# Kernel optimization log

Hardware: AMD Instinct MI355X
Metric: run time of the kernel (lower is better)

## Reference

```python
import jax, jax.numpy as jnp
import numpy as np

N_DOMAIN = 10
DOM_EMB = 4
IN_DIM = 1024
HIDDEN = [1024, 512, 256]
N_EXPERTS = 8
LORA_R = 16


def _glorot(key, shape):
    fan_in, fan_out = shape[-2], shape[-1]
    lim = np.sqrt(6.0 / (fan_in + fan_out))
    return jax.random.uniform(key, shape, jnp.float32, -lim, lim)


def setup_inputs() -> dict:
    key = jax.random.key(0)
    ks = jax.random.split(key, 32)
    inp = {
        "dnn_input": jax.random.normal(ks[0], (16384, IN_DIM), jnp.float32),
        "domain_input": jax.random.randint(ks[1], (16384,), 0, N_DOMAIN, jnp.int64),
        "emb_table": jax.random.normal(ks[2], (N_DOMAIN, DOM_EMB), jnp.float32),
        "gate_W": _glorot(ks[3], (DOM_EMB, N_EXPERTS)),
        "gate_b": jnp.zeros((N_EXPERTS,), jnp.float32),
    }
    prev = IN_DIM
    k = 4
    for li, h in enumerate(HIDDEN):
        inp[f"W{li}"] = _glorot(ks[k], (prev, h)); k += 1
        inp[f"b{li}"] = jnp.zeros((h,), jnp.float32)
        # original inits B and lora_bias to zeros; use small randoms so outputs/grads are non-trivial
        inp[f"A{li}"] = _glorot(ks[k], (N_EXPERTS, prev, LORA_R)); k += 1
        inp[f"B{li}"] = 0.01 * jax.random.normal(ks[k], (N_EXPERTS, LORA_R, h), jnp.float32); k += 1
        inp[f"lb{li}"] = 0.01 * jax.random.normal(ks[k], (N_EXPERTS, h), jnp.float32); k += 1
        prev = h
    return inp


def _moe_layer(x, gate, W, b, A, B, lb):
    # base GEMM (dropout is identity: rate 0 / inference)
    base = x @ W + b                                   # [B, h]
    t = jnp.einsum('bp,epr->ber', x, A)                # [B, E, r]
    eo = jnp.einsum('ber,erh->beh', t, B) + lb[None]   # [B, E, h]
    moe = jnp.einsum('be,beh->bh', gate, eo)           # [B, h]
    return jax.nn.relu(base + moe)


def reference(dnn_input, domain_input, emb_table, gate_W, gate_b,
              W0, b0, A0, B0, lb0,
              W1, b1, A1, B1, lb1,
              W2, b2, A2, B2, lb2):
    dom = emb_table[domain_input]                      # [B, 4]
    gate = jax.nn.softmax(dom @ gate_W + gate_b, axis=-1)  # [B, E]
    x = dnn_input
    x = _moe_layer(x, gate, W0, b0, A0, B0, lb0)
    x = _moe_layer(x, gate, W1, b1, A1, B1, lb1)
    x = _moe_layer(x, gate, W2, b2, A2, B2, lb2)
    return x
```

## Files before the change

### kernel.cpp

```cpp
#include <hip/hip_runtime.h>
#include <hip/hip_bf16.h>
#include <stdint.h>

#define KAUG 192
#define M_ROWS 16384

typedef __attribute__((ext_vector_type(8))) __bf16 bf16x8;
typedef __attribute__((ext_vector_type(4))) float f32x4;

__device__ __forceinline__ unsigned short f2b(float f) {
  unsigned int u = __builtin_bit_cast(unsigned int, f);
  u = (u + 0x7fffu + ((u >> 16) & 1u)) >> 16;
  return (unsigned short)u;
}

__device__ __forceinline__ void lds_load16(const unsigned short* g, unsigned short* l) {
  __builtin_amdgcn_global_load_lds(
      (const __attribute__((address_space(1))) void*)g,
      (__attribute__((address_space(3))) void*)l, 16, 0, 0);
}

template<int N> __device__ __forceinline__ void vmcnt_wait() {
  if constexpr (N == 0)      asm volatile("s_waitcnt vmcnt(0)" ::: "memory");
  else if constexpr (N == 3) asm volatile("s_waitcnt vmcnt(3)" ::: "memory");
  else if constexpr (N == 4) asm volatile("s_waitcnt vmcnt(4)" ::: "memory");
  else if constexpr (N == 6) asm volatile("s_waitcnt vmcnt(6)" ::: "memory");
  else                       asm volatile("s_waitcnt vmcnt(8)" ::: "memory");
}


__global__ void gate_aug_kernel(const int* __restrict__ dom, const float* __restrict__ emb,
                                const float* __restrict__ gW, const float* __restrict__ gb,
                                float* __restrict__ gate, unsigned short* __restrict__ tg) {
  int i = blockIdx.x * blockDim.x + threadIdx.x;
  int d = dom[i];
  float e0 = emb[d*4+0], e1 = emb[d*4+1], e2 = emb[d*4+2], e3 = emb[d*4+3];
  float l[8]; float mx = -1e30f;
#pragma unroll
  for (int j = 0; j < 8; j++) {
    l[j] = e0*gW[j] + e1*gW[8+j] + e2*gW[16+j] + e3*gW[24+j] + gb[j];
    mx = fmaxf(mx, l[j]);
  }
  float s = 0.f;
#pragma unroll
  for (int j = 0; j < 8; j++) { l[j] = __expf(l[j] - mx); s += l[j]; }
  float inv = 1.0f / s;
  unsigned int g[4];
#pragma unroll
  for (int j = 0; j < 8; j++) {
    float v = l[j] * inv;
    gate[i*8+j] = v;
    unsigned int b = f2b(v);
    if (j & 1) g[j >> 1] |= b << 16; else g[j >> 1] = b;
  }
  uint4* dst = (uint4*)&tg[(long)i * KAUG + 128];
  dst[0] = make_uint4(g[0], g[1], g[2], g[3]);
  uint4 z4 = make_uint4(0, 0, 0, 0);
#pragma unroll
  for (int q = 1; q < 8; q++) dst[q] = z4;
}

__global__ void build_wt_all(const float* __restrict__ w0, const float* __restrict__ w1,
                             const float* __restrict__ w2,
                             unsigned short* __restrict__ t0, unsigned short* __restrict__ t1,
                             unsigned short* __restrict__ t2) {
  int z = blockIdx.z;
  const float* W = z == 0 ? w0 : (z == 1 ? w1 : w2);
  unsigned short* Wt = z == 0 ? t0 : (z == 1 ? t1 : t2);
  int K = (z == 2) ? 512 : 1024;
  int N = (z == 0) ? 1024 : (z == 1 ? 512 : 256);
  int n0 = blockIdx.x * 32, k0 = blockIdx.y * 32;
  if (n0 >= N || k0 >= K) return;
  __shared__ float tl[32][33];
  int tx = threadIdx.x & 31, ty = threadIdx.x >> 5;
#pragma unroll
  for (int i = 0; i < 32; i += 8)
    tl[ty + i][tx] = W[(long)(k0 + ty + i) * N + n0 + tx];
  __syncthreads();
#pragma unroll
  for (int i = 0; i < 32; i += 8)
    Wt[(long)(n0 + ty + i) * K + k0 + tx] = f2b(tl[tx][ty + i]);
}

__global__ void build_aft_all(const float* __restrict__ a0, const float* __restrict__ a1,
                              const float* __restrict__ a2,
                              unsigned short* __restrict__ t0, unsigned short* __restrict__ t1,
                              unsigned short* __restrict__ t2) {
  int z = blockIdx.z;
  const float* A = z == 0 ? a0 : (z == 1 ? a1 : a2);
  unsigned short* Aft = z == 0 ? t0 : (z == 1 ? t1 : t2);
  int P = (z == 2) ? 512 : 1024;
  long p0 = (long)blockIdx.x * 64;
  if (p0 >= P) return;
  int e = blockIdx.y;
  __shared__ float tl[64][17];
  int t = threadIdx.x;
#pragma unroll
  for (int pass = 0; pass < 4; pass++) {
    int idx = t + pass * 256;
    int pl = idx >> 4, r = idx & 15;
    tl[pl][r] = A[((long)e * P + p0 + pl) * 16 + r];
  }
  __syncthreads();
#pragma unroll
  for (int pass = 0; pass < 4; pass++) {
    int idx = t + pass * 256;
    int r = idx >> 6, pl = idx & 63;
    Aft[(long)(e * 16 + r) * P + p0 + pl] = f2b(tl[pl][r]);
  }
}

__global__ void build_bft_all(const float* __restrict__ b0, const float* __restrict__ b1,
                              const float* __restrict__ b2,
                              const float* __restrict__ l0, const float* __restrict__ l1,
                              const float* __restrict__ l2,
                              unsigned short* __restrict__ t0, unsigned short* __restrict__ t1,
                              unsigned short* __restrict__ t2) {
  int z = blockIdx.z;
  const float* Bm = z == 0 ? b0 : (z == 1 ? b1 : b2);
  const float* lb = z == 0 ? l0 : (z == 1 ? l1 : l2);
  unsigned short* Bft = z == 0 ? t0 : (z == 1 ? t1 : t2);
  int H = (z == 0) ? 1024 : (z == 1 ? 512 : 256);
  int n0 = blockIdx.x * 32, kk0 = blockIdx.y * 32;
  if (n0 >= H) return;
  __shared__ float tl[32][33];
  int tx = threadIdx.x & 31, ty = threadIdx.x >> 5;
#pragma unroll
  for (int i = 0; i < 32; i += 8) {
    int kk = kk0 + ty + i;
    float v;
    if (kk < 128)       v = Bm[(long)kk * H + n0 + tx];
    else if (kk < 136)  v = lb[(long)(kk - 128) * H + n0 + tx];
    else                v = 0.f;
    tl[ty + i][tx] = v;
  }
  __syncthreads();
#pragma unroll
  for (int i = 0; i < 32; i += 8)
    Bft[(long)(n0 + ty + i) * KAUG + kk0 + tx] = f2b(tl[tx][ty + i]);
}

template<int MODE, int BM>
__global__ __launch_bounds__(512)
void gemm_mn(const unsigned short* __restrict__ A1, int lda1, int K1,
             const unsigned short* __restrict__ A2, int lda2, int K2,
             const unsigned short* __restrict__ Bt1, int ldb1,
             const unsigned short* __restrict__ Bt2, int ldb2,
             const float* __restrict__ bias,
             const float* __restrict__ gate,
             void* __restrict__ outp, int ldout) {
  constexpr int MFRAG = BM / 32;
  constexpr int ATOT = BM * 64;
  constexpr int BTOT = 128 * 64;
  constexpr int LA = BM / 64;
  constexpr int L = LA + 2;
  __shared__ __attribute__((aligned(16))) unsigned short lds[3 * ATOT + 3 * BTOT];

  const int t = threadIdx.x;
  const int lane = t & 63, wave = t >> 6;
  const int wr = wave >> 2, wc = wave & 3;
  const int rl = lane & 15, kg = lane >> 4;
  const int row0 = blockIdx.x * BM, col0 = blockIdx.y * 128;

  const int sr = t >> 3;
  const int sk = ((t & 7) ^ (sr & 7)) * 8;

  f32x4 acc[MFRAG][2];
#pragma unroll
  for (int m = 0; m < MFRAG; m++)
#pragma unroll
    for (int n = 0; n < 2; n++) acc[m][n] = (f32x4){0.f, 0.f, 0.f, 0.f};

  auto stageA = [&](int buf, int kt) {
    const unsigned short* src; long ld; int kl;
    if (kt < K1) { src = A1; ld = lda1; kl = kt; }
    else         { src = A2; ld = lda2; kl = kt - K1; }
    unsigned short* d = &lds[buf * ATOT + t * 8];
    const unsigned short* s = src + (long)(row0 + sr) * ld + kl + sk;
#pragma unroll
    for (int i = 0; i < LA; i++)
      lds_load16(s + (long)(i * 64) * ld, d + i * 4096);
  };
  auto stageB = [&](int buf, int kt) {
    const unsigned short* src; long ld; int kl;
    if (kt < K1) { src = Bt1; ld = ldb1; kl = kt; }
    else         { src = Bt2; ld = ldb2; kl = kt - K1; }
    unsigned short* d = &lds[3 * ATOT + buf * BTOT + t * 8];
    const unsigned short* s = src + (long)(col0 + sr) * ld + kl + sk;
    lds_load16(s, d);
    lds_load16(s + 64 * ld, d + 4096);
  };
  auto ldA = [&](int buf, int mg, int ks) {
    int lr = wr * (BM / 2) + mg * 16 + rl;
    int sc = (ks * 4 + kg) ^ (lr & 7);
    return *(const bf16x8*)&lds[buf * ATOT + lr * 64 + sc * 8];
  };
  auto ldB = [&](int buf, int n, int ks) {
    int cr = wc * 32 + n * 16 + rl;
    int sc = (ks * 4 + kg) ^ (cr & 7);
    return *(const bf16x8*)&lds[3 * ATOT + buf * BTOT + cr * 64 + sc * 8];
  };

  const int Ktot = K1 + K2;
  const int NT = Ktot / 64;

  stageA(0, 0); stageB(0, 0);
  stageA(1, 64); stageB(1, 64);
  vmcnt_wait<L>();
  __builtin_amdgcn_s_barrier();

  int bcur = 0;
  bf16x8 Bfv[2][2];
  for (int tt = 0; tt < NT; ++tt) {
    int bpf = bcur + 2; if (bpf > 2) bpf -= 3;
    const bool pf = (tt + 2 < NT);
    bf16x8 Af[(MFRAG + 1) / 2][2];
#pragma unroll
    for (int m = 0; m < MFRAG / 2; m++) { Af[m][0] = ldA(bcur, m, 0); Af[m][1] = ldA(bcur, m, 1); }
#pragma unroll
    for (int n = 0; n < 2; n++) { Bfv[n][0] = ldB(bcur, n, 0); Bfv[n][1] = ldB(bcur, n, 1); }
    if (pf) stageA(bpf, (tt + 2) * 64);
    __builtin_amdgcn_s_barrier();
    asm volatile("s_waitcnt lgkmcnt(0)" ::: "memory");
    __builtin_amdgcn_sched_barrier(0);
    __builtin_amdgcn_s_setprio(1);
#pragma unroll
    for (int m = 0; m < MFRAG / 2; m++)
#pragma unroll
      for (int n = 0; n < 2; n++) {
        acc[m][n] = __builtin_amdgcn_mfma_f32_16x16x32_bf16(Af[m][0], Bfv[n][0], acc[m][n], 0, 0, 0);
        acc[m][n] = __builtin_amdgcn_mfma_f32_16x16x32_bf16(Af[m][1], Bfv[n][1], acc[m][n], 0, 0, 0);
      }
    __builtin_amdgcn_s_setprio(0);
    __builtin_amdgcn_s_barrier();
#pragma unroll
    for (int m = 0; m < MFRAG / 2; m++) { Af[m][0] = ldA(bcur, MFRAG / 2 + m, 0); Af[m][1] = ldA(bcur, MFRAG / 2 + m, 1); }
    if (pf) stageB(bpf, (tt + 2) * 64);
    if (tt + 1 < NT) vmcnt_wait<L>();
    else             vmcnt_wait<0>();
    __builtin_amdgcn_s_barrier();
    asm volatile("s_waitcnt lgkmcnt(0)" ::: "memory");
    __builtin_amdgcn_sched_barrier(0);
    __builtin_amdgcn_s_setprio(1);
#pragma unroll
    for (int m = 0; m < MFRAG / 2; m++)
#pragma unroll
      for (int n = 0; n < 2; n++) {
        acc[MFRAG / 2 + m][n] = __builtin_amdgcn_mfma_f32_16x16x32_bf16(Af[m][0], Bfv[n][0], acc[MFRAG / 2 + m][n], 0, 0, 0);
        acc[MFRAG / 2 + m][n] = __builtin_amdgcn_mfma_f32_16x16x32_bf16(Af[m][1], Bfv[n][1], acc[MFRAG / 2 + m][n], 0, 0, 0);
      }
    __builtin_amdgcn_s_setprio(0);
    __builtin_amdgcn_s_barrier();
    bcur = bcur == 2 ? 0 : bcur + 1;
  }

#pragma unroll
  for (int m = 0; m < MFRAG; m++)
#pragma unroll
    for (int n = 0; n < 2; n++)
#pragma unroll
      for (int j = 0; j < 4; j++) {
        int row = row0 + wr * (BM / 2) + m * 16 + kg * 4 + j;
        int col = col0 + wc * 32 + n * 16 + rl;
        float v = acc[m][n][j];
        if (MODE == 0) {
          v *= gate[row * 8 + (col >> 4)];
          ((unsigned short*)outp)[(long)row * ldout + col] = f2b(v);
        } else {
          v += bias[col];
          v = fmaxf(v, 0.f);
          if (MODE == 1) ((unsigned short*)outp)[(long)row * ldout + col] = f2b(v);
          else           ((float*)outp)[(long)row * ldout + col] = v;
        }
      }
}

template<int MODE, int BM, bool F32A>
__global__ __launch_bounds__(256, F32A ? 2 : 4)
void gemm2b(const unsigned short* __restrict__ A1, int lda1, int K1,
            const unsigned short* __restrict__ A2, int lda2, int K2,
            const unsigned short* __restrict__ Bt1, int ldb1,
            const unsigned short* __restrict__ Bt2, int ldb2,
            const float* __restrict__ bias,
            const float* __restrict__ gate,
            void* __restrict__ outp, int ldout,
            const float* __restrict__ Af32) {
  constexpr int ATOT = BM * 64;
  constexpr int BTOT = 128 * 64;
  constexpr int MF = BM / 64;
  constexpr int LA = BM / 32;
  __shared__ __attribute__((aligned(16))) unsigned short lds[2 * ATOT + 2 * BTOT];

  const int t = threadIdx.x;
  const int lane = t & 63, wave = t >> 6;
  const int wr = wave >> 1, wc = wave & 1;
  const int rl = lane & 15, kg = lane >> 4;
  const int row0 = blockIdx.x * BM, col0 = blockIdx.y * 128;

  const int sr = t >> 3;
  const int sk = ((t & 7) ^ (sr & 7)) * 8;

  f32x4 acc[2 * MF][4];
#pragma unroll
  for (int m = 0; m < 2 * MF; m++)
#pragma unroll
    for (int n = 0; n < 4; n++) acc[m][n] = (f32x4){0.f, 0.f, 0.f, 0.f};

  auto stageA = [&](int buf, int kt) {
    unsigned short* d = &lds[buf * ATOT + t * 8];
    if constexpr (F32A) {
      if (kt < K1) {
        const float* s = Af32 + (long)(row0 + sr) * lda1 + kt + sk;
#pragma unroll
        for (int i = 0; i < LA; i++) {
          const float* sp = s + (long)(i * 32) * lda1;
          float4 a = *(const float4*)sp;
          float4 b = *(const float4*)(sp + 4);
          uint4 o;
          o.x = f2b(a.x) | ((unsigned)f2b(a.y) << 16);
          o.y = f2b(a.z) | ((unsigned)f2b(a.w) << 16);
          o.z = f2b(b.x) | ((unsigned)f2b(b.y) << 16);
          o.w = f2b(b.z) | ((unsigned)f2b(b.w) << 16);
          *(uint4*)(d + i * 2048) = o;
        }
        return;
      }
    }
    const unsigned short* src; long ld; int kl;
    if (kt < K1) { src = A1; ld = lda1; kl = kt; }
    else         { src = A2; ld = lda2; kl = kt - K1; }
    const unsigned short* s = src + (long)(row0 + sr) * ld + kl + sk;
#pragma unroll
    for (int i = 0; i < LA; i++)
      lds_load16(s + (long)(i * 32) * ld, d + i * 2048);
  };
  auto stageB = [&](int buf, int kt) {
    const unsigned short* src; long ld; int kl;
    if (kt < K1) { src = Bt1; ld = ldb1; kl = kt; }
    else         { src = Bt2; ld = ldb2; kl = kt - K1; }
    unsigned short* d = &lds[2 * ATOT + buf * BTOT + t * 8];
    const unsigned short* s = src + (long)(col0 + sr) * ld + kl + sk;
#pragma unroll
    for (int i = 0; i < 4; i++)
      lds_load16(s + (long)(i * 32) * ld, d + i * 2048);
  };
  auto ldA = [&](int buf, int mf, int ks) {
    int lr = wr * (BM / 2) + mf * 16 + rl;
    int sc = (ks * 4 + kg) ^ (lr & 7);
    return *(const bf16x8*)&lds[buf * ATOT + lr * 64 + sc * 8];
  };
  auto ldB = [&](int buf, int nf, int ks) {
    int cr = wc * 64 + nf * 16 + rl;
    int sc = (ks * 4 + kg) ^ (cr & 7);
    return *(const bf16x8*)&lds[2 * ATOT + buf * BTOT + cr * 64 + sc * 8];
  };

  const int NT = (K1 + K2) / 64;

  stageA(0, 0); stageB(0, 0);
  __syncthreads();

  int cur = 0;
  for (int tt = 0; tt < NT; ++tt) {
    const bool pf = (tt + 1 < NT);
    const int kt1 = (tt + 1) * 64;
    if (pf) { stageA(cur ^ 1, kt1); stageB(cur ^ 1, kt1); }
    bf16x8 Am_[MF][2], Bf[4][2];
#pragma unroll
    for (int mf = 0; mf < MF; mf++) { Am_[mf][0] = ldA(cur, mf, 0); Am_[mf][1] = ldA(cur, mf, 1); }
#pragma unroll
    for (int nf = 0; nf < 4; nf++) { Bf[nf][0] = ldB(cur, nf, 0); Bf[nf][1] = ldB(cur, nf, 1); }
    asm volatile("s_waitcnt lgkmcnt(0)" ::: "memory");
    __builtin_amdgcn_sched_barrier(0);
    __builtin_amdgcn_s_setprio(1);
#pragma unroll
    for (int mf = 0; mf < MF; mf++)
#pragma unroll
      for (int nf = 0; nf < 4; nf++) {
        acc[mf][nf] = __builtin_amdgcn_mfma_f32_16x16x32_bf16(Am_[mf][0], Bf[nf][0], acc[mf][nf], 0, 0, 0);
        acc[mf][nf] = __builtin_amdgcn_mfma_f32_16x16x32_bf16(Am_[mf][1], Bf[nf][1], acc[mf][nf], 0, 0, 0);
      }
    __builtin_amdgcn_s_setprio(0);
#pragma unroll
    for (int mf = 0; mf < MF; mf++) { Am_[mf][0] = ldA(cur, MF + mf, 0); Am_[mf][1] = ldA(cur, MF + mf, 1); }
    asm volatile("s_waitcnt lgkmcnt(0)" ::: "memory");
    __builtin_amdgcn_sched_barrier(0);
    __builtin_amdgcn_s_setprio(1);
#pragma unroll
    for (int mf = 0; mf < MF; mf++)
#pragma unroll
      for (int nf = 0; nf < 4; nf++) {
        acc[MF + mf][nf] = __builtin_amdgcn_mfma_f32_16x16x32_bf16(Am_[mf][0], Bf[nf][0], acc[MF + mf][nf], 0, 0, 0);
        acc[MF + mf][nf] = __builtin_amdgcn_mfma_f32_16x16x32_bf16(Am_[mf][1], Bf[nf][1], acc[MF + mf][nf], 0, 0, 0);
      }
    __builtin_amdgcn_s_setprio(0);
    if constexpr (F32A) {
      __syncthreads();
    } else {
      if (pf) asm volatile("s_waitcnt vmcnt(0)" ::: "memory");
      __builtin_amdgcn_s_barrier();
    }
    cur ^= 1;
  }

#pragma unroll
  for (int m = 0; m < 2 * MF; m++)
#pragma unroll
    for (int n = 0; n < 4; n++)
#pragma unroll
      for (int j = 0; j < 4; j++) {
        int row = row0 + wr * (BM / 2) + m * 16 + kg * 4 + j;
        int col = col0 + wc * 64 + n * 16 + rl;
        float v = acc[m][n][j];
        if (MODE == 0) {
          v *= gate[row * 8 + (col >> 4)];
          ((unsigned short*)outp)[(long)row * ldout + col] = f2b(v);
        } else {
          v += bias[col];
          v = fmaxf(v, 0.f);
          if (MODE == 1) ((unsigned short*)outp)[(long)row * ldout + col] = f2b(v);
          else           ((float*)outp)[(long)row * ldout + col] = v;
        }
      }
}


extern "C" void kernel_launch(void* const* d_in, const int* in_sizes, int n_in,
                              void* d_out, int out_size, void* d_ws, size_t ws_size,
                              hipStream_t stream) {
  (void)in_sizes; (void)n_in; (void)out_size; (void)ws_size;
  const float* dnn = (const float*)d_in[0];
  const int*   dom = (const int*)d_in[1];
  const float* emb = (const float*)d_in[2];
  const float* gW  = (const float*)d_in[3];
  const float* gb  = (const float*)d_in[4];
  const float* Wm[3]  = {(const float*)d_in[5],  (const float*)d_in[10], (const float*)d_in[15]};
  const float* bm[3]  = {(const float*)d_in[6],  (const float*)d_in[11], (const float*)d_in[16]};
  const float* Am[3]  = {(const float*)d_in[7],  (const float*)d_in[12], (const float*)d_in[17]};
  const float* Bm[3]  = {(const float*)d_in[8],  (const float*)d_in[13], (const float*)d_in[18]};
  const float* lbm[3] = {(const float*)d_in[9],  (const float*)d_in[14], (const float*)d_in[19]};

  const int M = M_ROWS;
  const int dIn[3]  = {1024, 1024, 512};
  const int dOutN[3] = {1024, 512, 256};

  char* p = (char*)d_ws;
  auto carve = [&](size_t bytes) { char* r = p; p += (bytes + 255) & ~(size_t)255; return r; };
  float* gate = (float*)carve((size_t)M * 8 * sizeof(float));
  unsigned short* xb0 = (unsigned short*)carve((size_t)M * 1024 * 2);
  unsigned short* xb1 = (unsigned short*)carve((size_t)M * 1024 * 2);
  unsigned short* tg  = (unsigned short*)carve((size_t)M * KAUG * 2);
  unsigned short *Wt[3], *Aft[3], *Bft[3];
  for (int l = 0; l < 3; l++) {
    Wt[l]  = (unsigned short*)carve((size_t)dOutN[l] * dIn[l] * 2);
    Aft[l] = (unsigned short*)carve((size_t)128 * dIn[l] * 2);
    Bft[l] = (unsigned short*)carve((size_t)dOutN[l] * KAUG * 2);
  }

  gate_aug_kernel<<<M / 256, 256, 0, stream>>>(dom, emb, gW, gb, gate, tg);
  build_wt_all<<<dim3(32, 32, 3), 256, 0, stream>>>(Wm[0], Wm[1], Wm[2], Wt[0], Wt[1], Wt[2]);
  build_aft_all<<<dim3(16, 8, 3), 256, 0, stream>>>(Am[0], Am[1], Am[2], Aft[0], Aft[1], Aft[2]);
  build_bft_all<<<dim3(32, KAUG / 32, 3), 256, 0, stream>>>(Bm[0], Bm[1], Bm[2],
                                                            lbm[0], lbm[1], lbm[2],
                                                            Bft[0], Bft[1], Bft[2]);

  gemm2b<0, 64, true><<<dim3(M / 64, 1), 256, 0, stream>>>(
      nullptr, 1024, 1024, nullptr, 0, 0, Aft[0], 1024, nullptr, 0,
      nullptr, gate, (void*)tg, KAUG, dnn);
  gemm2b<1, 128, true><<<dim3(M / 128, 1024 / 128), 256, 0, stream>>>(
      nullptr, 1024, 1024, tg, KAUG, KAUG, Wt[0], 1024, Bft[0], KAUG,
      bm[0], nullptr, (void*)xb1, 1024, dnn);
  gemm_mn<0, 64><<<dim3(M / 64, 1), 512, 0, stream>>>(
      xb1, 1024, 1024, nullptr, 0, 0, Aft[1], 1024, nullptr, 0, nullptr, gate, (void*)tg, KAUG);
  gemm2b<1, 128, false><<<dim3(M / 128, 512 / 128), 256, 0, stream>>>(
      xb1, 1024, 1024, tg, KAUG, KAUG, Wt[1], 1024, Bft[1], KAUG,
      bm[1], nullptr, (void*)xb0, 512, nullptr);
  gemm_mn<0, 64><<<dim3(M / 64, 1), 512, 0, stream>>>(
      xb0, 512, 512, nullptr, 0, 0, Aft[2], 512, nullptr, 0, nullptr, gate, (void*)tg, KAUG);
  gemm2b<2, 64, false><<<dim3(M / 64, 256 / 128), 256, 0, stream>>>(
      xb0, 512, 512, tg, KAUG, KAUG, Wt[2], 512, Bft[2], KAUG,
      bm[2], nullptr, d_out, 256, nullptr);
}
```

Baseline: 153.3 us.

## Emit bf16 copy of input in LoRA-down GEMM and software-pipeline fp32 A loads

The first LoRA-down GEMM now writes the bf16-converted input rows to a workspace buffer while staging them. This lets the layer-0 main GEMM read bf16 through async global-to-LDS loads instead of re-reading and converting fp32 data in each of 8 column blocks. The fp32 staging is also split into an issue phase before the MFMAs and a convert-and-commit phase after them, so load latency overlaps compute. The cost is an extra 32MB bf16 write in the first kernel and more registers held across the MFMA loop.

New measurement: 142.2 us. -7.3%, faster.

```diff
diff --git a/kernel.cpp b/kernel.cpp
--- a/kernel.cpp
+++ b/kernel.cpp
@@ -284,7 +284,8 @@
             const float* __restrict__ bias,
             const float* __restrict__ gate,
             void* __restrict__ outp, int ldout,
-            const float* __restrict__ Af32) {
+            const float* __restrict__ Af32,
+            unsigned short* __restrict__ xout) {
   constexpr int ATOT = BM * 64;
   constexpr int BTOT = 128 * 64;
   constexpr int MF = BM / 64;
@@ -306,29 +307,35 @@
 #pragma unroll
     for (int n = 0; n < 4; n++) acc[m][n] = (f32x4){0.f, 0.f, 0.f, 0.f};
 
+  float4 ra[LA], rb[LA];
+
+  auto stageA_issue = [&](int kt) {
+    const float* s = Af32 + (long)(row0 + sr) * lda1 + kt + sk;
+#pragma unroll
+    for (int i = 0; i < LA; i++) {
+      const float* sp = s + (long)(i * 32) * lda1;
+      ra[i] = *(const float4*)sp;
+      rb[i] = *(const float4*)(sp + 4);
+    }
+  };
+  auto stageA_commit = [&](int buf, int kt) {
+    unsigned short* d = &lds[buf * ATOT + t * 8];
+#pragma unroll
+    for (int i = 0; i < LA; i++) {
+      uint4 o;
+      o.x = f2b(ra[i].x) | ((unsigned)f2b(ra[i].y) << 16);
+      o.y = f2b(ra[i].z) | ((unsigned)f2b(ra[i].w) << 16);
+      o.z = f2b(rb[i].x) | ((unsigned)f2b(rb[i].y) << 16);
+      o.w = f2b(rb[i].z) | ((unsigned)f2b(rb[i].w) << 16);
+      *(uint4*)(d + i * 2048) = o;
+      *(uint4*)&xout[(long)(row0 + sr + i * 32) * lda1 + kt + sk] = o;
+    }
+  };
   auto stageA = [&](int buf, int kt) {
-    unsigned short* d = &lds[buf * ATOT + t * 8];
-    if constexpr (F32A) {
-      if (kt < K1) {
-        const float* s = Af32 + (long)(row0 + sr) * lda1 + kt + sk;
-#pragma unroll
-        for (int i = 0; i < LA; i++) {
-          const float* sp = s + (long)(i * 32) * lda1;
-          float4 a = *(const float4*)sp;
-          float4 b = *(const float4*)(sp + 4);
-          uint4 o;
-          o.x = f2b(a.x) | ((unsigned)f2b(a.y) << 16);
-          o.y = f2b(a.z) | ((unsigned)f2b(a.w) << 16);
-          o.z = f2b(b.x) | ((unsigned)f2b(b.y) << 16);
-          o.w = f2b(b.z) | ((unsigned)f2b(b.w) << 16);
-          *(uint4*)(d + i * 2048) = o;
-        }
-        return;
-      }
-    }
     const unsigned short* src; long ld; int kl;
     if (kt < K1) { src = A1; ld = lda1; kl = kt; }
     else         { src = A2; ld = lda2; kl = kt - K1; }
+    unsigned short* d = &lds[buf * ATOT + t * 8];
     const unsigned short* s = src + (long)(row0 + sr) * ld + kl + sk;
 #pragma unroll
     for (int i = 0; i < LA; i++)
@@ -357,14 +364,30 @@
 
   const int NT = (K1 + K2) / 64;
 
-  stageA(0, 0); stageB(0, 0);
-  __syncthreads();
+  if constexpr (F32A) {
+    stageA_issue(0); stageB(0, 0);
+    stageA_commit(0, 0);
+    __syncthreads();
+  } else {
+    stageA(0, 0); stageB(0, 0);
+    asm volatile("s_waitcnt vmcnt(0)" ::: "memory");
+    __builtin_amdgcn_s_barrier();
+  }
 
   int cur = 0;
   for (int tt = 0; tt < NT; ++tt) {
     const bool pf = (tt + 1 < NT);
     const int kt1 = (tt + 1) * 64;
-    if (pf) { stageA(cur ^ 1, kt1); stageB(cur ^ 1, kt1); }
+    bool f32next = false;
+    if (pf) {
+      if constexpr (F32A) {
+        if (kt1 < K1) { stageA_issue(kt1); f32next = true; }
+        else          stageA(cur ^ 1, kt1);
+      } else {
+        stageA(cur ^ 1, kt1);
+      }
+      stageB(cur ^ 1, kt1);
+    }
     bf16x8 Am_[MF][2], Bf[4][2];
 #pragma unroll
     for (int mf = 0; mf < MF; mf++) { Am_[mf][0] = ldA(cur, mf, 0); Am_[mf][1] = ldA(cur, mf, 1); }
@@ -395,6 +418,7 @@
       }
     __builtin_amdgcn_s_setprio(0);
     if constexpr (F32A) {
+      if (f32next) stageA_commit(cur ^ 1, kt1);
       __syncthreads();
     } else {
       if (pf) asm volatile("s_waitcnt vmcnt(0)" ::: "memory");
@@ -441,8 +465,6 @@
   const float* lbm[3] = {(const float*)d_in[9],  (const float*)d_in[14], (const float*)d_in[19]};
 
   const int M = M_ROWS;
-  const int dIn[3]  = {1024, 1024, 512};
-  const int dOutN[3] = {1024, 512, 256};
 
   char* p = (char*)d_ws;
   auto carve = [&](size_t bytes) { char* r = p; p += (bytes + 255) & ~(size_t)255; return r; };
@@ -450,6 +472,8 @@
   unsigned short* xb0 = (unsigned short*)carve((size_t)M * 1024 * 2);
   unsigned short* xb1 = (unsigned short*)carve((size_t)M * 1024 * 2);
   unsigned short* tg  = (unsigned short*)carve((size_t)M * KAUG * 2);
+  const int dIn[3]  = {1024, 1024, 512};
+  const int dOutN[3] = {1024, 512, 256};
   unsigned short *Wt[3], *Aft[3], *Bft[3];
   for (int l = 0; l < 3; l++) {
     Wt[l]  = (unsigned short*)carve((size_t)dOutN[l] * dIn[l] * 2);
@@ -466,18 +490,18 @@
 
   gemm2b<0, 64, true><<<dim3(M / 64, 1), 256, 0, stream>>>(
       nullptr, 1024, 1024, nullptr, 0, 0, Aft[0], 1024, nullptr, 0,
-      nullptr, gate, (void*)tg, KAUG, dnn);
-  gemm2b<1, 128, true><<<dim3(M / 128, 1024 / 128), 256, 0, stream>>>(
-      nullptr, 1024, 1024, tg, KAUG, KAUG, Wt[0], 1024, Bft[0], KAUG,
-      bm[0], nullptr, (void*)xb1, 1024, dnn);
+      nullptr, gate, (void*)tg, KAUG, dnn, xb0);
+  gemm2b<1, 128, false><<<dim3(M / 128, 1024 / 128), 256, 0, stream>>>(
+      xb0, 1024, 1024, tg, KAUG, KAUG, Wt[0], 1024, Bft[0], KAUG,
+      bm[0], nullptr, (void*)xb1, 1024, nullptr, nullptr);
   gemm_mn<0, 64><<<dim3(M / 64, 1), 512, 0, stream>>>(
       xb1, 1024, 1024, nullptr, 0, 0, Aft[1], 1024, nullptr, 0, nullptr, gate, (void*)tg, KAUG);
   gemm2b<1, 128, false><<<dim3(M / 128, 512 / 128), 256, 0, stream>>>(
       xb1, 1024, 1024, tg, KAUG, KAUG, Wt[1], 1024, Bft[1], KAUG,
-      bm[1], nullptr, (void*)xb0, 512, nullptr);
+      bm[1], nullptr, (void*)xb0, 512, nullptr, nullptr);
   gemm_mn<0, 64><<<dim3(M / 64, 1), 512, 0, stream>>>(
       xb0, 512, 512, nullptr, 0, 0, Aft[2], 512, nullptr, 0, nullptr, gate, (void*)tg, KAUG);
   gemm2b<2, 64, false><<<dim3(M / 64, 256 / 128), 256, 0, stream>>>(
       xb0, 512, 512, tg, KAUG, KAUG, Wt[2], 512, Bft[2], KAUG,
-      bm[2], nullptr, d_out, 256, nullptr);
-}
+      bm[2], nullptr, d_out, 256, nullptr, nullptr);
+}
```
